# Kernel tuning notes

Hardware: AMD Instinct MI355X
Metric: run time of the kernel (lower is better)

## Reference

```python
import jax, jax.numpy as jnp
import numpy as np

N = 100000
E = 1600000
F_IN = 128
F_HID = 128


def gcn_conv(x, src, dst, deg_inv_sqrt, W, b, n_nodes):
    # x: [N, Fin] -> [N, Fout]; symmetric-normalized aggregation with self-loops
    h = x @ W  # [N, Fout]
    norm = deg_inv_sqrt[src] * deg_inv_sqrt[dst]  # [E+N] (self-loops appended)
    msgs = h[src] * norm[:, None]  # [E+N, Fout]
    out = jax.ops.segment_sum(msgs, dst, num_segments=n_nodes)
    return out + b


def setup_inputs() -> dict:
    key = jax.random.key(0)
    k = jax.random.split(key, 8)
    x = jax.random.normal(k[0], (N, F_IN), dtype=jnp.float32)
    edge_index = jax.random.randint(k[1], (2, E), 0, N, dtype=jnp.int32)
    s = 1.0 / np.sqrt(F_IN)
    W1 = jax.random.uniform(k[2], (F_IN, F_HID), jnp.float32, -s, s)
    b1 = jnp.zeros((F_HID,), jnp.float32)
    s2 = 1.0 / np.sqrt(F_HID)
    W2 = jax.random.uniform(k[3], (F_HID, F_HID), jnp.float32, -s2, s2)
    b2 = jnp.zeros((F_HID,), jnp.float32)
    W3 = jax.random.uniform(k[4], (F_HID, 1), jnp.float32, -s2, s2)
    b3 = jnp.zeros((1,), jnp.float32)
    return {"x": x, "edge_index": edge_index, "W1": W1, "b1": b1,
            "W2": W2, "b2": b2, "W3": W3, "b3": b3}


def reference(x, edge_index, W1, b1, W2, b2, W3, b3):
    n = x.shape[0]
    loops = jnp.arange(n, dtype=edge_index.dtype)
    src = jnp.concatenate([edge_index[0], loops])  # add self-loops
    dst = jnp.concatenate([edge_index[1], loops])
    deg = jax.ops.segment_sum(jnp.ones_like(dst, dtype=x.dtype), dst, num_segments=n)
    deg_inv_sqrt = jnp.where(deg > 0, jax.lax.rsqrt(deg), 0.0)

    h = gcn_conv(x, src, dst, deg_inv_sqrt, W1, b1, n)
    h = jax.nn.relu(h)  # dropout is identity at inference
    h = gcn_conv(h, src, dst, deg_inv_sqrt, W2, b2, n)
    h = jax.nn.relu(h)
    h = gcn_conv(h, src, dst, deg_inv_sqrt, W3, b3, n)
    return jax.nn.sigmoid(h)  # [N, 1]
```

## Files before the change

### kernel.cpp

```cpp
#include <hip/hip_runtime.h>
#include <cstdint>
#include <cstddef>

#define NN 100000
#define NE 1600000
#define FD 128
#define NXCD 8
#define RNODES ((NN + NXCD - 1) / NXCD)

__device__ __forceinline__ float bf_lo(uint32_t u) { return __uint_as_float(u << 16); }
__device__ __forceinline__ float bf_hi(uint32_t u) { return __uint_as_float(u & 0xffff0000u); }
__device__ __forceinline__ uint32_t bf_pack(float a, float b) {
    uint32_t ua = __float_as_uint(a), ub = __float_as_uint(b);
    ua += 0x7fffu + ((ua >> 16) & 1u);
    ub += 0x7fffu + ((ub >> 16) & 1u);
    return (ua >> 16) | (ub & 0xffff0000u);
}

__global__ __launch_bounds__(256) void k_hist(const int* __restrict__ dst,
                                              int* __restrict__ cnt, int e) {
    const int xcd   = blockIdx.x & 7;
    const int chunk = blockIdx.x >> 3;
    const int lo = xcd * RNODES;
    const int hi = lo + RNODES;
    const int base = chunk * 1024 + threadIdx.x * 4;
    if (base >= e) return;
    int4 d4 = *(const int4*)(dst + base);
    #pragma unroll
    for (int j = 0; j < 4; ++j) {
        int d = (&d4.x)[j];
        if (d >= lo && d < hi) atomicAdd(&cnt[d], 1);
    }
}

__global__ __launch_bounds__(1024) void k_scan1(const int* __restrict__ cnt,
                                                int* __restrict__ excl,
                                                int* __restrict__ bsum, int n) {
    __shared__ int sh[1024];
    int i = blockIdx.x * 1024 + threadIdx.x;
    int v = (i < n) ? cnt[i] : 0;
    sh[threadIdx.x] = v;
    __syncthreads();
    for (int off = 1; off < 1024; off <<= 1) {
        int t = (threadIdx.x >= off) ? sh[threadIdx.x - off] : 0;
        __syncthreads();
        sh[threadIdx.x] += t;
        __syncthreads();
    }
    if (i < n) excl[i] = sh[threadIdx.x] - v;
    if (threadIdx.x == 1023) bsum[blockIdx.x] = sh[1023];
}

__global__ void k_scan2(int* __restrict__ bsum, int nb) {
    __shared__ int sh[128];
    int t = threadIdx.x;
    int v = (t < nb) ? bsum[t] : 0;
    sh[t] = v;
    __syncthreads();
    for (int off = 1; off < 128; off <<= 1) {
        int u = (t >= off) ? sh[t - off] : 0;
        __syncthreads();
        sh[t] += u;
        __syncthreads();
    }
    if (t < nb) bsum[t] = sh[t] - v;
}

__global__ void k_scan3(int* __restrict__ excl, const int* __restrict__ bsum,
                        int* __restrict__ cursor, const int* __restrict__ cnt,
                        float* __restrict__ dis, int n, int e) {
    int i = blockIdx.x * blockDim.x + threadIdx.x;
    if (i < n) {
        int v = excl[i] + bsum[i >> 10];
        excl[i] = v;
        cursor[i] = v;
        dis[i] = rsqrtf((float)(cnt[i] + 1));
    }
    if (i == 0) excl[n] = e;
}

__global__ __launch_bounds__(256) void k_fill(const int* __restrict__ src,
                                              const int* __restrict__ dst,
                                              int* __restrict__ cursor,
                                              int* __restrict__ col,
                                              float* __restrict__ wedge,
                                              const float* __restrict__ dis, int e) {
    const int xcd   = blockIdx.x & 7;
    const int chunk = blockIdx.x >> 3;
    const int lo = xcd * RNODES;
    const int hi = lo + RNODES;
    const int base = chunk * 1024 + threadIdx.x * 4;
    if (base >= e) return;
    int4 d4 = *(const int4*)(dst + base);
    #pragma unroll
    for (int j = 0; j < 4; ++j) {
        int d = (&d4.x)[j];
        if (d >= lo && d < hi) {
            int s   = src[base + j];
            int pos = atomicAdd(&cursor[d], 1);
            col[pos]   = s;
            wedge[pos] = dis[s] * dis[d];
        }
    }
}

template <typename TIN>
__global__ __launch_bounds__(256) void k_gemm(const TIN* __restrict__ X,
                                              const float* __restrict__ W,
                                              unsigned short* __restrict__ H, int n) {
    __shared__ float At[64][68];
    __shared__ float Ws[64][64];
    const int t  = threadIdx.x;
    const int tx = t & 15;
    const int ty = t >> 4;
    const int rb = blockIdx.x * 64;
    const int cb = blockIdx.y * 64;

    float acc[4][4] = {};

    for (int c = 0; c < 2; ++c) {
        #pragma unroll
        for (int r = 0; r < 4; ++r) {
            int f   = t + 256 * r;
            int row = f >> 4;
            int kc  = (f & 15) << 2;
            int grow = rb + row;
            float4 v = make_float4(0.f, 0.f, 0.f, 0.f);
            if (grow < n) {
                if constexpr (sizeof(TIN) == 4) {
                    v = *(const float4*)((const float*)X + (size_t)grow * FD + c * 64 + kc);
                } else {
                    uint2 p = *(const uint2*)((const unsigned short*)X + (size_t)grow * FD + c * 64 + kc);
                    v.x = bf_lo(p.x); v.y = bf_hi(p.x);
                    v.z = bf_lo(p.y); v.w = bf_hi(p.y);
                }
            }
            At[kc + 0][row] = v.x;
            At[kc + 1][row] = v.y;
            At[kc + 2][row] = v.z;
            At[kc + 3][row] = v.w;
            *(float4*)&Ws[row][kc] =
                *(const float4*)(W + (size_t)(c * 64 + row) * FD + cb + kc);
        }
        __syncthreads();
        #pragma unroll 8
        for (int k = 0; k < 64; ++k) {
            float4 a = *(const float4*)&At[k][ty * 4];
            float4 b = *(const float4*)&Ws[k][tx * 4];
            acc[0][0] = fmaf(a.x, b.x, acc[0][0]);
            acc[0][1] = fmaf(a.x, b.y, acc[0][1]);
            acc[0][2] = fmaf(a.x, b.z, acc[0][2]);
            acc[0][3] = fmaf(a.x, b.w, acc[0][3]);
            acc[1][0] = fmaf(a.y, b.x, acc[1][0]);
            acc[1][1] = fmaf(a.y, b.y, acc[1][1]);
            acc[1][2] = fmaf(a.y, b.z, acc[1][2]);
            acc[1][3] = fmaf(a.y, b.w, acc[1][3]);
            acc[2][0] = fmaf(a.z, b.x, acc[2][0]);
            acc[2][1] = fmaf(a.z, b.y, acc[2][1]);
            acc[2][2] = fmaf(a.z, b.z, acc[2][2]);
            acc[2][3] = fmaf(a.z, b.w, acc[2][3]);
            acc[3][0] = fmaf(a.w, b.x, acc[3][0]);
            acc[3][1] = fmaf(a.w, b.y, acc[3][1]);
            acc[3][2] = fmaf(a.w, b.z, acc[3][2]);
            acc[3][3] = fmaf(a.w, b.w, acc[3][3]);
        }
        __syncthreads();
    }

    #pragma unroll
    for (int i = 0; i < 4; ++i) {
        int grow = rb + ty * 4 + i;
        if (grow < n) {
            uint2 p;
            p.x = bf_pack(acc[i][0], acc[i][1]);
            p.y = bf_pack(acc[i][2], acc[i][3]);
            *(uint2*)(H + (size_t)grow * FD + cb + tx * 4) = p;
        }
    }
}

template <int MODE>
__global__ __launch_bounds__(256) void k_agg(const unsigned short* __restrict__ h,
                                             const float* __restrict__ dis,
                                             const int* __restrict__ rp,
                                             const int* __restrict__ col,
                                             const float* __restrict__ wedge,
                                             const float* __restrict__ bias,
                                             const float* __restrict__ W3,
                                             unsigned short* __restrict__ out,
                                             float* __restrict__ outf, int n) {
    const uint32_t* h32 = (const uint32_t*)h;
    int wid  = (int)((blockIdx.x * (size_t)blockDim.x + threadIdx.x) >> 6);
    int lane = threadIdx.x & 63;
    int w2 = __builtin_amdgcn_readfirstlane(wid);
    int i0 = 2 * w2;
    if (i0 >= n) return;
    int i1 = i0 + 1;
    const bool has1 = (i1 < n);

    const int e00 = rp[i0];
    const int e01 = rp[i0 + 1];
    const int e11 = has1 ? rp[i0 + 2] : e01;

    float di0 = dis[i0];
    float di1 = has1 ? dis[i1] : 0.f;
    float2 acc0, acc1;
    {
        uint32_t su0 = h32[(size_t)i0 * 64 + lane];
        float q0 = di0 * di0;
        acc0.x = bf_lo(su0) * q0; acc0.y = bf_hi(su0) * q0;
        if (has1) {
            uint32_t su1 = h32[(size_t)i1 * 64 + lane];
            float q1 = di1 * di1;
            acc1.x = bf_lo(su1) * q1; acc1.y = bf_hi(su1) * q1;
        } else { acc1.x = acc1.y = 0.f; }
    }

    const int ng0 = (e01 - e00 + 15) >> 4;
    const int ng1 = (e11 - e01 + 15) >> 4;
    const int ng  = ng0 > ng1 ? ng0 : ng1;

    for (int g = 0; g < ng; ++g) {
        const bool do0 = (g < ng0), do1 = (g < ng1);
        int s0[16], s1[16];
        float w0_[16], w1_[16];
        uint32_t v0[16], v1[16];
        if (do0) {
            const int jb = e00 + g * 16;
            #pragma unroll
            for (int q = 0; q < 16; ++q) {
                int idx = jb + q;
                int c   = idx < e01 ? idx : e01 - 1;
                s0[q]  = col[c];
                w0_[q] = idx < e01 ? wedge[c] : 0.f;
            }
        }
        if (do1) {
            const int jb = e01 + g * 16;
            #pragma unroll
            for (int q = 0; q < 16; ++q) {
                int idx = jb + q;
                int c   = idx < e11 ? idx : e11 - 1;
                s1[q]  = col[c];
                w1_[q] = idx < e11 ? wedge[c] : 0.f;
            }
        }
        if (do0) {
            #pragma unroll
            for (int q = 0; q < 16; ++q)
                v0[q] = h32[(size_t)s0[q] * 64 + lane];
        }
        if (do1) {
            #pragma unroll
            for (int q = 0; q < 16; ++q)
                v1[q] = h32[(size_t)s1[q] * 64 + lane];
        }
        if (do0) {
            #pragma unroll
            for (int q = 0; q < 16; ++q) {
                acc0.x = fmaf(w0_[q], bf_lo(v0[q]), acc0.x);
                acc0.y = fmaf(w0_[q], bf_hi(v0[q]), acc0.y);
            }
        }
        if (do1) {
            #pragma unroll
            for (int q = 0; q < 16; ++q) {
                acc1.x = fmaf(w1_[q], bf_lo(v1[q]), acc1.x);
                acc1.y = fmaf(w1_[q], bf_hi(v1[q]), acc1.y);
            }
        }
    }

    float2 b = ((const float2*)bias)[lane];
    acc0.x = fmaxf(acc0.x + b.x, 0.f);
    acc0.y = fmaxf(acc0.y + b.y, 0.f);
    acc1.x = fmaxf(acc1.x + b.x, 0.f);
    acc1.y = fmaxf(acc1.y + b.y, 0.f);

    if (MODE == 0) {
        ((uint32_t*)out)[(size_t)i0 * 64 + lane] = bf_pack(acc0.x, acc0.y);
        if (has1)
            ((uint32_t*)out)[(size_t)i1 * 64 + lane] = bf_pack(acc1.x, acc1.y);
    } else {
        float2 w3 = ((const float2*)W3)[lane];
        float d0 = acc0.x * w3.x + acc0.y * w3.y;
        float d1 = acc1.x * w3.x + acc1.y * w3.y;
        #pragma unroll
        for (int off = 32; off; off >>= 1) {
            d0 += __shfl_xor(d0, off);
            d1 += __shfl_xor(d1, off);
        }
        if (lane == 0) {
            outf[i0] = d0;
            if (has1) outf[i1] = d1;
        }
    }
}

__global__ __launch_bounds__(256) void k_agg1(const float* __restrict__ h3,
                                              const float* __restrict__ dis,
                                              const int* __restrict__ rp,
                                              const int* __restrict__ col,
                                              const float* __restrict__ wedge,
                                              const float* __restrict__ b3,
                                              float* __restrict__ out, int n) {
    int i    = (int)((blockIdx.x * (size_t)blockDim.x + threadIdx.x) >> 6);
    int lane = threadIdx.x & 63;
    if (i >= n) return;
    float di  = dis[i];
    float acc = (lane == 0) ? di * di * h3[i] : 0.f;
    const int e0 = rp[i], e1 = rp[i + 1];
    for (int base = e0 + lane; base < e1; base += 64) {
        acc = fmaf(wedge[base], h3[col[base]], acc);
    }
    #pragma unroll
    for (int off = 32; off; off >>= 1) acc += __shfl_xor(acc, off);
    if (lane == 0) {
        float v = acc + b3[0];
        out[i] = 1.f / (1.f + expf(-v));
    }
}

static inline size_t alg(size_t x) { return (x + 255) & ~(size_t)255; }

extern "C" void kernel_launch(void* const* d_in, const int* in_sizes, int n_in,
                              void* d_out, int out_size, void* d_ws, size_t ws_size,
                              hipStream_t stream) {
    const float* x   = (const float*)d_in[0];
    const int*   ei  = (const int*)d_in[1];
    const float* W1  = (const float*)d_in[2];
    const float* b1  = (const float*)d_in[3];
    const float* W2  = (const float*)d_in[4];
    const float* b2  = (const float*)d_in[5];
    const float* W3  = (const float*)d_in[6];
    const float* b3  = (const float*)d_in[7];
    float*       out = (float*)d_out;

    const int n = NN, e = NE;
    const int* src = ei;
    const int* dst = ei + e;

    char* w = (char*)d_ws;
    float* dis    = (float*)w;  w += alg((size_t)n * 4);
    int*   cnt    = (int*)w;    w += alg((size_t)n * 4);
    int*   rp     = (int*)w;    w += alg((size_t)(n + 1) * 4);
    int*   cursor = (int*)w;    w += alg((size_t)n * 4);
    int*   bsum   = (int*)w;    w += alg((size_t)128 * 4);
    int*   col    = (int*)w;    w += alg((size_t)e * 4);
    float* wedge  = (float*)w;  w += alg((size_t)e * 4);
    unsigned short* bufA = (unsigned short*)w; w += alg((size_t)n * FD * 2);
    unsigned short* bufB = (unsigned short*)w; w += alg((size_t)n * FD * 2);
    float* h3     = (float*)w;  w += alg((size_t)n * 4);

    hipMemsetAsync(cnt, 0, (size_t)n * 4, stream);

    const int B = 256;
    const int gN = (n + B - 1) / B;
    const int nScan = (n + 1023) / 1024;
    const int nChunk = (e + 1023) / 1024;

    k_hist<<<nChunk * NXCD, B, 0, stream>>>(dst, cnt, e);
    k_scan1<<<nScan, 1024, 0, stream>>>(cnt, rp, bsum, n);
    k_scan2<<<1, 128, 0, stream>>>(bsum, nScan);
    k_scan3<<<gN, B, 0, stream>>>(rp, bsum, cursor, cnt, dis, n, e);
    k_fill<<<nChunk * NXCD, B, 0, stream>>>(src, dst, cursor, col, wedge, dis, e);

    dim3 gGemm((n + 63) / 64, 2);
    const int nWave2  = (n + 1) / 2;
    const int gWave2  = (nWave2 * 64 + B - 1) / B;
    const int gWave   = (n * 64 + B - 1) / B;

    k_gemm<float><<<gGemm, B, 0, stream>>>(x, W1, bufA, n);
    k_agg<0><<<gWave2, B, 0, stream>>>(bufA, dis, rp, col, wedge, b1, W3, bufB, h3, n);
    k_gemm<unsigned short><<<gGemm, B, 0, stream>>>(bufB, W2, bufA, n);
    k_agg<1><<<gWave2, B, 0, stream>>>(bufA, dis, rp, col, wedge, b2, W3, bufB, h3, n);
    k_agg1<<<gWave, B, 0, stream>>>(h3, dis, rp, col, wedge, b3, out, n);
}
```

Baseline: 517.6 us.

## Interleave CSR column and edge weight into one array, add nontemporal edge loads

```diff
diff --git a/kernel.cpp b/kernel.cpp
--- a/kernel.cpp
+++ b/kernel.cpp
@@ -7,6 +7,8 @@
 #define FD 128
 #define NXCD 8
 #define RNODES ((NN + NXCD - 1) / NXCD)
+
+typedef int vi4 __attribute__((ext_vector_type(4)));
 
 __device__ __forceinline__ float bf_lo(uint32_t u) { return __uint_as_float(u << 16); }
 __device__ __forceinline__ float bf_hi(uint32_t u) { return __uint_as_float(u & 0xffff0000u); }
@@ -25,10 +27,10 @@
     const int hi = lo + RNODES;
     const int base = chunk * 1024 + threadIdx.x * 4;
     if (base >= e) return;
-    int4 d4 = *(const int4*)(dst + base);
+    vi4 d4 = __builtin_nontemporal_load((const vi4*)(dst + base));
     #pragma unroll
     for (int j = 0; j < 4; ++j) {
-        int d = (&d4.x)[j];
+        int d = d4[j];
         if (d >= lo && d < hi) atomicAdd(&cnt[d], 1);
     }
 }
@@ -82,8 +84,7 @@
 __global__ __launch_bounds__(256) void k_fill(const int* __restrict__ src,
                                               const int* __restrict__ dst,
                                               int* __restrict__ cursor,
-                                              int* __restrict__ col,
-                                              float* __restrict__ wedge,
+                                              uint2* __restrict__ colw,
                                               const float* __restrict__ dis, int e) {
     const int xcd   = blockIdx.x & 7;
     const int chunk = blockIdx.x >> 3;
@@ -91,15 +92,18 @@
     const int hi = lo + RNODES;
     const int base = chunk * 1024 + threadIdx.x * 4;
     if (base >= e) return;
-    int4 d4 = *(const int4*)(dst + base);
+    vi4 d4 = __builtin_nontemporal_load((const vi4*)(dst + base));
+    vi4 s4 = __builtin_nontemporal_load((const vi4*)(src + base));
     #pragma unroll
     for (int j = 0; j < 4; ++j) {
-        int d = (&d4.x)[j];
+        int d = d4[j];
         if (d >= lo && d < hi) {
-            int s   = src[base + j];
+            int s   = s4[j];
             int pos = atomicAdd(&cursor[d], 1);
-            col[pos]   = s;
-            wedge[pos] = dis[s] * dis[d];
+            uint2 cw;
+            cw.x = (uint32_t)s;
+            cw.y = __float_as_uint(dis[s] * dis[d]);
+            colw[pos] = cw;
         }
     }
 }
@@ -183,8 +187,7 @@
 __global__ __launch_bounds__(256) void k_agg(const unsigned short* __restrict__ h,
                                              const float* __restrict__ dis,
                                              const int* __restrict__ rp,
-                                             const int* __restrict__ col,
-                                             const float* __restrict__ wedge,
+                                             const uint2* __restrict__ colw,
                                              const float* __restrict__ bias,
                                              const float* __restrict__ W3,
                                              unsigned short* __restrict__ out,
@@ -227,22 +230,40 @@
         uint32_t v0[16], v1[16];
         if (do0) {
             const int jb = e00 + g * 16;
-            #pragma unroll
-            for (int q = 0; q < 16; ++q) {
-                int idx = jb + q;
-                int c   = idx < e01 ? idx : e01 - 1;
-                s0[q]  = col[c];
-                w0_[q] = idx < e01 ? wedge[c] : 0.f;
+            if (jb + 16 <= e01) {
+                #pragma unroll
+                for (int q = 0; q < 16; ++q) {
+                    uint2 cw = colw[jb + q];
+                    s0[q] = (int)cw.x; w0_[q] = __uint_as_float(cw.y);
+                }
+            } else {
+                #pragma unroll
+                for (int q = 0; q < 16; ++q) {
+                    int idx = jb + q;
+                    int c   = idx < e01 ? idx : e01 - 1;
+                    uint2 cw = colw[c];
+                    s0[q]  = (int)cw.x;
+                    w0_[q] = idx < e01 ? __uint_as_float(cw.y) : 0.f;
+                }
             }
         }
         if (do1) {
             const int jb = e01 + g * 16;
-            #pragma unroll
-            for (int q = 0; q < 16; ++q) {
-                int idx = jb + q;
-                int c   = idx < e11 ? idx : e11 - 1;
-                s1[q]  = col[c];
-                w1_[q] = idx < e11 ? wedge[c] : 0.f;
+            if (jb + 16 <= e11) {
+                #pragma unroll
+                for (int q = 0; q < 16; ++q) {
+                    uint2 cw = colw[jb + q];
+                    s1[q] = (int)cw.x; w1_[q] = __uint_as_float(cw.y);
+                }
+            } else {
+                #pragma unroll
+                for (int q = 0; q < 16; ++q) {
+                    int idx = jb + q;
+                    int c   = idx < e11 ? idx : e11 - 1;
+                    uint2 cw = colw[c];
+                    s1[q]  = (int)cw.x;
+                    w1_[q] = idx < e11 ? __uint_as_float(cw.y) : 0.f;
+                }
             }
         }
         if (do0) {
@@ -300,8 +321,7 @@
 __global__ __launch_bounds__(256) void k_agg1(const float* __restrict__ h3,
                                               const float* __restrict__ dis,
                                               const int* __restrict__ rp,
-                                              const int* __restrict__ col,
-                                              const float* __restrict__ wedge,
+                                              const uint2* __restrict__ colw,
                                               const float* __restrict__ b3,
                                               float* __restrict__ out, int n) {
     int i    = (int)((blockIdx.x * (size_t)blockDim.x + threadIdx.x) >> 6);
@@ -311,7 +331,8 @@
     float acc = (lane == 0) ? di * di * h3[i] : 0.f;
     const int e0 = rp[i], e1 = rp[i + 1];
     for (int base = e0 + lane; base < e1; base += 64) {
-        acc = fmaf(wedge[base], h3[col[base]], acc);
+        uint2 cw = colw[base];
+        acc = fmaf(__uint_as_float(cw.y), h3[(int)cw.x], acc);
     }
     #pragma unroll
     for (int off = 32; off; off >>= 1) acc += __shfl_xor(acc, off);
@@ -346,8 +367,7 @@
     int*   rp     = (int*)w;    w += alg((size_t)(n + 1) * 4);
     int*   cursor = (int*)w;    w += alg((size_t)n * 4);
     int*   bsum   = (int*)w;    w += alg((size_t)128 * 4);
-    int*   col    = (int*)w;    w += alg((size_t)e * 4);
-    float* wedge  = (float*)w;  w += alg((size_t)e * 4);
+    uint2* colw   = (uint2*)w;  w += alg((size_t)e * 8);
     unsigned short* bufA = (unsigned short*)w; w += alg((size_t)n * FD * 2);
     unsigned short* bufB = (unsigned short*)w; w += alg((size_t)n * FD * 2);
     float* h3     = (float*)w;  w += alg((size_t)n * 4);
@@ -363,7 +383,7 @@
     k_scan1<<<nScan, 1024, 0, stream>>>(cnt, rp, bsum, n);
     k_scan2<<<1, 128, 0, stream>>>(bsum, nScan);
     k_scan3<<<gN, B, 0, stream>>>(rp, bsum, cursor, cnt, dis, n, e);
-    k_fill<<<nChunk * NXCD, B, 0, stream>>>(src, dst, cursor, col, wedge, dis, e);
+    k_fill<<<nChunk * NXCD, B, 0, stream>>>(src, dst, cursor, colw, dis, e);
 
     dim3 gGemm((n + 63) / 64, 2);
     const int nWave2  = (n + 1) / 2;
@@ -371,8 +391,8 @@
     const int gWave   = (n * 64 + B - 1) / B;
 
     k_gemm<float><<<gGemm, B, 0, stream>>>(x, W1, bufA, n);
-    k_agg<0><<<gWave2, B, 0, stream>>>(bufA, dis, rp, col, wedge, b1, W3, bufB, h3, n);
+    k_agg<0><<<gWave2, B, 0, stream>>>(bufA, dis, rp, colw, b1, W3, bufB, h3, n);
     k_gemm<unsigned short><<<gGemm, B, 0, stream>>>(bufB, W2, bufA, n);
-    k_agg<1><<<gWave2, B, 0, stream>>>(bufA, dis, rp, col, wedge, b2, W3, bufB, h3, n);
-    k_agg1<<<gWave, B, 0, stream>>>(h3, dis, rp, col, wedge, b3, out, n);
-}
+    k_agg<1><<<gWave2, B, 0, stream>>>(bufA, dis, rp, colw, b2, W3, bufB, h3, n);
+    k_agg1<<<gWave, B, 0, stream>>>(h3, dis, rp, colw, b3, out, n);
+}
```

Measured after the change: 531.4 us. +2.7%, slower.
